# Kernel tuning notes

Measured on AMD Instinct MI355X. Metric: run time of the kernel, lower is better.

Reference implementation:

```python
import jax, jax.numpy as jnp
import numpy as np

N, E, D_IN = 50000, 800000, 64
EMB = [128, 128, 128, 128]
LIN = [128, 64]
B = 512  # number of graphs
BN_EPS = 1e-5


def setup_inputs() -> dict:
    key = jax.random.key(0)
    ks = jax.random.split(key, 20)
    inp = {
        "x": jax.random.normal(ks[0], (N, D_IN), dtype=jnp.float32),
        "edge_index": jax.random.randint(ks[1], (2, E), 0, N, dtype=jnp.int32),
        "batch_index": jnp.sort(jax.random.randint(ks[2], (N,), 0, B, dtype=jnp.int32)),
    }
    dims = [D_IN] + EMB
    for i in range(4):
        s = 1.0 / np.sqrt(dims[i])
        inp[f"W{i+1}"] = jax.random.uniform(ks[3 + i], (dims[i], dims[i + 1]), jnp.float32, -s, s)
        inp[f"b{i+1}"] = jnp.zeros((dims[i + 1],), jnp.float32)
    inp["lW1"] = jax.random.uniform(ks[8], (EMB[-1], LIN[0]), jnp.float32, -0.08, 0.08)
    inp["lb1"] = jnp.zeros((LIN[0],), jnp.float32)
    inp["lW2"] = jax.random.uniform(ks[9], (LIN[0], LIN[1]), jnp.float32, -0.08, 0.08)
    inp["lb2"] = jnp.zeros((LIN[1],), jnp.float32)
    inp["gamma"] = jnp.ones((LIN[1],), jnp.float32)
    inp["beta"] = jnp.zeros((LIN[1],), jnp.float32)
    inp["running_mean"] = jnp.zeros((LIN[1],), jnp.float32)
    inp["running_var"] = jnp.ones((LIN[1],), jnp.float32)
    inp["oW"] = jax.random.uniform(ks[10], (LIN[1], 1), jnp.float32, -0.12, 0.12)
    inp["ob"] = jnp.zeros((1,), jnp.float32)
    return inp


def reference(x, edge_index, batch_index, W1, b1, W2, b2, W3, b3, W4, b4,
              lW1, lb1, lW2, lb2, gamma, beta, running_mean, running_var, oW, ob):
    n = x.shape[0]
    loop = jnp.arange(n, dtype=edge_index.dtype)
    src = jnp.concatenate([edge_index[0], loop])  # [E+N]
    dst = jnp.concatenate([edge_index[1], loop])
    # GCN symmetric normalization (PyG GCNConv: deg from target with self-loops)
    deg = jax.ops.segment_sum(jnp.ones_like(dst, x.dtype), dst, num_segments=n)
    dinv = jnp.where(deg > 0, jax.lax.rsqrt(deg), 0.0)
    norm = dinv[src] * dinv[dst]  # [E+N]

    def conv(h, W, b):
        h = h @ W                                   # [N, out]
        msg = h[src] * norm[:, None]                # gather per edge
        return jax.ops.segment_sum(msg, dst, num_segments=n) + b

    h = jax.nn.relu(conv(x, W1, b1))
    h = jax.nn.relu(conv(h, W2, b2))
    h = jax.nn.relu(conv(h, W3, b3))
    h = jax.nn.relu(conv(h, W4, b4))

    # global mean pool over graphs (dropout layers are identity in eval mode)
    sums = jax.ops.segment_sum(h, batch_index, num_segments=B)
    cnts = jax.ops.segment_sum(jnp.ones((n,), h.dtype), batch_index, num_segments=B)
    pooled = sums / jnp.maximum(cnts, 1.0)[:, None]  # [B, EMB[-1]]

    h = pooled @ lW1 + lb1
    h = h @ lW2 + lb2
    h = (h - running_mean) * gamma * jax.lax.rsqrt(running_var + BN_EPS) + beta
    hidden = jax.nn.relu(h)
    out = hidden @ oW + ob
    return (out, hidden)
```

## Files before the change

kernel.cpp:

```cpp
#include <hip/hip_runtime.h>
#include <hip/hip_fp16.h>

struct alignas(8) half4v { __half2 a, b; };
using f16x8 = __attribute__((ext_vector_type(8))) _Float16;
using f32x4 = __attribute__((ext_vector_type(4))) float;

__global__ void zero_kernel(int* __restrict__ p, int n) {
  int i = blockIdx.x * blockDim.x + threadIdx.x;
  if (i < n) p[i] = 0;
}

__global__ void hist_kernel(const int* __restrict__ dst, int* __restrict__ deg,
                            int* __restrict__ eidx, int E) {
  int e0 = (blockIdx.x * blockDim.x + threadIdx.x) * 4;
  if (e0 + 3 < E) {
    int4 d4 = *(const int4*)&dst[e0];
    int r0 = atomicAdd(&deg[d4.x], 1);
    int r1 = atomicAdd(&deg[d4.y], 1);
    int r2 = atomicAdd(&deg[d4.z], 1);
    int r3 = atomicAdd(&deg[d4.w], 1);
    int4 o; o.x = r0; o.y = r1; o.z = r2; o.w = r3;
    *(int4*)&eidx[e0] = o;
  } else {
    for (int e = e0; e < E; ++e) eidx[e] = atomicAdd(&deg[dst[e]], 1);
  }
}

__global__ void dinv_bsum_kernel(const int* __restrict__ deg, float* __restrict__ dinv,
                                 int* __restrict__ bsum, int n) {
  __shared__ int s[256];
  int i = blockIdx.x * 256 + threadIdx.x;
  int d = (i < n) ? deg[i] : 0;
  if (i < n) dinv[i] = rsqrtf((float)(d + 1));
  s[threadIdx.x] = d;
  __syncthreads();
  for (int off = 128; off > 0; off >>= 1) {
    if (threadIdx.x < off) s[threadIdx.x] += s[threadIdx.x + off];
    __syncthreads();
  }
  if (threadIdx.x == 0) bsum[blockIdx.x] = s[0];
}

__global__ void scan_bsum_kernel(const int* __restrict__ bsum, int* __restrict__ bexcl,
                                 int nb, int* __restrict__ rowptr_last) {
  __shared__ int s[256];
  int t = threadIdx.x;
  int v = (t < nb) ? bsum[t] : 0;
  s[t] = v;
  __syncthreads();
  for (int off = 1; off < 256; off <<= 1) {
    int add = (t >= off) ? s[t - off] : 0;
    __syncthreads();
    s[t] += add;
    __syncthreads();
  }
  if (t < nb) bexcl[t] = s[t] - v;
  if (t == 255) *rowptr_last = s[255];
}

__global__ void rowptr_kernel(const int* __restrict__ cnt, const int* __restrict__ bexcl,
                              int* __restrict__ rowptr, int n) {
  __shared__ int s[256];
  int i = blockIdx.x * 256 + threadIdx.x;
  int t = threadIdx.x;
  int v = (i < n) ? cnt[i] : 0;
  s[t] = v;
  __syncthreads();
  for (int off = 1; off < 256; off <<= 1) {
    int add = (t >= off) ? s[t - off] : 0;
    __syncthreads();
    s[t] += add;
    __syncthreads();
  }
  if (i < n) rowptr[i] = bexcl[blockIdx.x] + s[t] - v;
}

__global__ void fill_kernel(const int* __restrict__ src, const int* __restrict__ dst,
                            const float* __restrict__ dinv, const int* __restrict__ rowptr,
                            const int* __restrict__ eidx, int2* __restrict__ colwv, int E) {
  int e0 = (blockIdx.x * blockDim.x + threadIdx.x) * 2;
  if (e0 + 1 < E) {
    int2 s2 = *(const int2*)&src[e0];
    int2 d2 = *(const int2*)&dst[e0];
    int2 x2 = *(const int2*)&eidx[e0];
    float dsx = dinv[s2.x], ddx = dinv[d2.x];
    float dsy = dinv[s2.y], ddy = dinv[d2.y];
    int slot0 = rowptr[d2.x] + x2.x;
    int slot1 = rowptr[d2.y] + x2.y;
    int2 p0; p0.x = s2.x; p0.y = __float_as_int(dsx * ddx);
    int2 p1; p1.x = s2.y; p1.y = __float_as_int(dsy * ddy);
    colwv[slot0] = p0;
    colwv[slot1] = p1;
  } else if (e0 < E) {
    int s = src[e0], d = dst[e0];
    int slot = rowptr[d] + eidx[e0];
    int2 packed;
    packed.x = s;
    packed.y = __float_as_int(dinv[s] * dinv[d]);
    colwv[slot] = packed;
  }
}

__global__ void f32_to_f16_kernel(const float* __restrict__ in, __half* __restrict__ out,
                                  int total4) {
  int i = blockIdx.x * blockDim.x + threadIdx.x;
  if (i >= total4) return;
  float4 v = ((const float4*)in)[i];
  half4v o;
  o.a = __floats2half2_rn(v.x, v.y);
  o.b = __floats2half2_rn(v.z, v.w);
  ((half4v*)out)[i] = o;
}

__global__ void pack_w_all_kernel(const float* __restrict__ W1, __half* __restrict__ Wp1,
                                  const float* __restrict__ W2, __half* __restrict__ Wp2,
                                  const float* __restrict__ W3, __half* __restrict__ Wp3,
                                  const float* __restrict__ W4, __half* __restrict__ Wp4) {
  int b = blockIdx.x;
  const float* W; __half* Wp; int idx;
  if (b < 32)       { W = W1; Wp = Wp1; idx = b * 256 + threadIdx.x; }
  else if (b < 96)  { W = W2; Wp = Wp2; idx = (b - 32) * 256 + threadIdx.x; }
  else if (b < 160) { W = W3; Wp = Wp3; idx = (b - 96) * 256 + threadIdx.x; }
  else              { W = W4; Wp = Wp4; idx = (b - 160) * 256 + threadIdx.x; }
  int j = idx & 7;
  int lane = (idx >> 3) & 63;
  int c = (idx >> 9) & 7;
  int ks = idx >> 12;
  int k = ks * 32 + ((lane >> 4) << 3) + j;
  int col = c * 16 + (lane & 15);
  Wp[idx] = __float2half(W[k * 128 + col]);
}

template <int D>
__global__ __launch_bounds__(256) void aggregate_h_kernel(
    const __half* __restrict__ h, const int* __restrict__ rowptr,
    const int2* __restrict__ colwv, const float* __restrict__ dinv,
    __half* __restrict__ out, int n) {
  int wid = (blockIdx.x * 256 + threadIdx.x) >> 6;
  int lane = threadIdx.x & 63;
  if (wid >= n) return;
  float di = dinv[wid];
  float sl = di * di;
  int beg = rowptr[wid], end = rowptr[wid + 1];
  const half4v* h4 = (const half4v*)h;
  constexpr int RQ = D / 4;
  float4 acc = {0.f, 0.f, 0.f, 0.f};
  constexpr int EPG = (D == 128) ? 2 : 4;
  const int sub = (D == 128) ? (lane >> 5) : (lane >> 4);
  const int lq = (D == 128) ? (lane & 31) : (lane & 15);
  for (int base = beg; base < end; base += 64) {
    int kk = base + lane;
    int c = 0; float ww = 0.f;
    if (kk < end) { int2 e = colwv[kk]; c = e.x; ww = __int_as_float(e.y); }
    int m = end - base; if (m > 64) m = 64;
    for (int t0 = 0; t0 < m; t0 += 8 * EPG) {
      half4v v[8]; float ws[8];
      #pragma unroll
      for (int u = 0; u < 8; ++u) {
        int t = t0 + EPG * u + sub;
        int cs = __shfl(c, t);
        ws[u] = __shfl(ww, t);
        v[u] = h4[(size_t)cs * RQ + lq];
      }
      #pragma unroll
      for (int u = 0; u < 8; ++u) {
        float2 fa = __half22float2(v[u].a);
        float2 fb = __half22float2(v[u].b);
        acc.x += ws[u] * fa.x; acc.y += ws[u] * fa.y;
        acc.z += ws[u] * fb.x; acc.w += ws[u] * fb.y;
      }
    }
  }
  if constexpr (D == 64) {
    acc.x += __shfl_xor(acc.x, 16); acc.y += __shfl_xor(acc.y, 16);
    acc.z += __shfl_xor(acc.z, 16); acc.w += __shfl_xor(acc.w, 16);
  }
  acc.x += __shfl_xor(acc.x, 32); acc.y += __shfl_xor(acc.y, 32);
  acc.z += __shfl_xor(acc.z, 32); acc.w += __shfl_xor(acc.w, 32);
  if (lane < RQ) {
    half4v hv = h4[(size_t)wid * RQ + lane];
    float2 fa = __half22float2(hv.a);
    float2 fb = __half22float2(hv.b);
    acc.x += sl * fa.x; acc.y += sl * fa.y; acc.z += sl * fb.x; acc.w += sl * fb.y;
    half4v o;
    o.a = __floats2half2_rn(acc.x, acc.y);
    o.b = __floats2half2_rn(acc.z, acc.w);
    ((half4v*)out)[(size_t)wid * RQ + lane] = o;
  }
}

template <int K>
__global__ __launch_bounds__(256) void gemm_mfma_kernel(
    const __half* __restrict__ A, const __half* __restrict__ Wp,
    const float* __restrict__ bias, __half* __restrict__ C, int n) {
  const int wave = threadIdx.x >> 6;
  const int lane = threadIdx.x & 63;
  const int r0 = blockIdx.x * 64 + wave * 16;
  const int arow = r0 + (lane & 15);
  const int kgrp = lane >> 4;
  f32x4 acc[8] = {};
  const f16x8* Wp8 = (const f16x8*)Wp;
  #pragma unroll
  for (int ks = 0; ks < K / 32; ++ks) {
    f16x8 afrag = {};
    if (arow < n) afrag = *(const f16x8*)&A[(size_t)arow * K + ks * 32 + kgrp * 8];
    #pragma unroll
    for (int c = 0; c < 8; ++c) {
      f16x8 bfrag = Wp8[(ks * 8 + c) * 64 + lane];
      acc[c] = __builtin_amdgcn_mfma_f32_16x16x32_f16(afrag, bfrag, acc[c], 0, 0, 0);
    }
  }
  const int colbase = lane & 15;
  #pragma unroll
  for (int c = 0; c < 8; ++c) {
    int col = c * 16 + colbase;
    float bv = bias[col];
    #pragma unroll
    for (int j = 0; j < 4; ++j) {
      int row = r0 + kgrp * 4 + j;
      if (row < n) C[(size_t)row * 128 + col] = __float2half(fmaxf(acc[c][j] + bv, 0.f));
    }
  }
}

__global__ __launch_bounds__(256) void pool_mean_kernel(
    const __half* __restrict__ h, const int* __restrict__ batch,
    float* __restrict__ pooled, int n) {
  int b = blockIdx.x;
  int lo = 0, hi = n;
  while (lo < hi) { int mid = (lo + hi) >> 1; if (batch[mid] < b) lo = mid + 1; else hi = mid; }
  int s = lo;
  hi = n;
  while (lo < hi) { int mid = (lo + hi) >> 1; if (batch[mid] < b + 1) lo = mid + 1; else hi = mid; }
  int e = lo;
  const half4v* h4 = (const half4v*)h;
  int q = threadIdx.x & 31;
  int r = threadIdx.x >> 5;
  float4 acc = {0.f, 0.f, 0.f, 0.f};
  for (int i = s + r; i < e; i += 8) {
    half4v v = h4[(size_t)i * 32 + q];
    float2 fa = __half22float2(v.a), fb = __half22float2(v.b);
    acc.x += fa.x; acc.y += fa.y; acc.z += fb.x; acc.w += fb.y;
  }
  __shared__ float4 red[8][32];
  red[r][q] = acc;
  __syncthreads();
  for (int off = 4; off > 0; off >>= 1) {
    if (r < off) {
      float4 o = red[r + off][q];
      acc.x += o.x; acc.y += o.y; acc.z += o.z; acc.w += o.w;
      red[r][q] = acc;
    }
    __syncthreads();
  }
  if (r == 0) {
    float c = fmaxf((float)(e - s), 1.0f);
    float4 o;
    o.x = acc.x / c; o.y = acc.y / c; o.z = acc.z / c; o.w = acc.w / c;
    ((float4*)pooled)[b * 32 + q] = o;
  }
}

__global__ __launch_bounds__(128) void mlp_kernel(
    const float* __restrict__ pooled,
    const float* __restrict__ lW1, const float* __restrict__ lb1,
    const float* __restrict__ lW2, const float* __restrict__ lb2,
    const float* __restrict__ gamma, const float* __restrict__ beta,
    const float* __restrict__ rm, const float* __restrict__ rv,
    const float* __restrict__ oW, const float* __restrict__ ob,
    float* __restrict__ out, int B) {
  int b = blockIdx.x, t = threadIdx.x;
  __shared__ float p[128], h1[128];
  p[t] = pooled[b * 128 + t];
  __syncthreads();
  float a1 = lb1[t];
  for (int k = 0; k < 128; ++k) a1 += p[k] * lW1[k * 128 + t];
  h1[t] = a1;
  __syncthreads();
  if (t < 64) {
    float a2 = lb2[t];
    for (int k = 0; k < 128; ++k) a2 += h1[k] * lW2[k * 64 + t];
    a2 = (a2 - rm[t]) * gamma[t] * rsqrtf(rv[t] + 1e-5f) + beta[t];
    float hd = fmaxf(a2, 0.f);
    out[B + b * 64 + t] = hd;
    float prod = hd * oW[t];
    #pragma unroll
    for (int off = 32; off > 0; off >>= 1) prod += __shfl_down(prod, off);
    if (t == 0) out[b] = prod + ob[0];
  }
}

extern "C" void kernel_launch(void* const* d_in, const int* in_sizes, int n_in,
                              void* d_out, int out_size, void* d_ws, size_t ws_size,
                              hipStream_t stream) {
  const float* x = (const float*)d_in[0];
  const int* ei = (const int*)d_in[1];
  const int* batch = (const int*)d_in[2];
  const float* W1 = (const float*)d_in[3];  const float* b1 = (const float*)d_in[4];
  const float* W2 = (const float*)d_in[5];  const float* b2 = (const float*)d_in[6];
  const float* W3 = (const float*)d_in[7];  const float* b3 = (const float*)d_in[8];
  const float* W4 = (const float*)d_in[9];  const float* b4 = (const float*)d_in[10];
  const float* lW1 = (const float*)d_in[11]; const float* lb1 = (const float*)d_in[12];
  const float* lW2 = (const float*)d_in[13]; const float* lb2 = (const float*)d_in[14];
  const float* gamma = (const float*)d_in[15]; const float* beta = (const float*)d_in[16];
  const float* rm = (const float*)d_in[17]; const float* rv = (const float*)d_in[18];
  const float* oW = (const float*)d_in[19]; const float* ob = (const float*)d_in[20];

  const int n = in_sizes[2];
  const int E = in_sizes[1] / 2;
  const int B = out_size / 65;
  const int* src = ei;
  const int* dst = ei + E;

  char* ws = (char*)d_ws;
  size_t off = 0;
  auto alloc = [&](size_t bytes) -> void* {
    void* p = ws + off;
    off += (bytes + 255) & ~(size_t)255;
    return p;
  };
  int* deg = (int*)alloc((size_t)n * 4);
  float* dinv = (float*)alloc((size_t)n * 4);
  int* rowptr = (int*)alloc((size_t)(n + 1) * 4);
  int* eidx = (int*)alloc((size_t)E * 4);
  int* bsum = (int*)alloc(256 * 4);
  int* bexcl = (int*)alloc(256 * 4);
  int2* colwv = (int2*)alloc((size_t)E * 8);
  __half* aggh = (__half*)alloc((size_t)n * 128 * 2);
  __half* hbuf = (__half*)alloc((size_t)n * 128 * 2);
  __half* xh = (__half*)alloc((size_t)n * 64 * 2);
  __half* Wp1 = (__half*)alloc(64 * 128 * 2);
  __half* Wp2 = (__half*)alloc(128 * 128 * 2);
  __half* Wp3 = (__half*)alloc(128 * 128 * 2);
  __half* Wp4 = (__half*)alloc(128 * 128 * 2);
  float* pooled = (float*)alloc((size_t)B * 128 * 4);

  const int nb = (n + 255) / 256;
  zero_kernel<<<nb, 256, 0, stream>>>(deg, n);
  hist_kernel<<<(E / 4 + 255) / 256, 256, 0, stream>>>(dst, deg, eidx, E);
  f32_to_f16_kernel<<<(n * 16 + 255) / 256, 256, 0, stream>>>(x, xh, n * 16);
  pack_w_all_kernel<<<224, 256, 0, stream>>>(W1, Wp1, W2, Wp2, W3, Wp3, W4, Wp4);
  dinv_bsum_kernel<<<nb, 256, 0, stream>>>(deg, dinv, bsum, n);
  scan_bsum_kernel<<<1, 256, 0, stream>>>(bsum, bexcl, nb, rowptr + n);
  rowptr_kernel<<<nb, 256, 0, stream>>>(deg, bexcl, rowptr, n);
  fill_kernel<<<(E / 2 + 255) / 256, 256, 0, stream>>>(src, dst, dinv, rowptr, eidx, colwv, E);

  const int aggblocks = (n + 3) / 4;
  const int gemmblocks = (n + 63) / 64;

  aggregate_h_kernel<64><<<aggblocks, 256, 0, stream>>>(xh, rowptr, colwv, dinv, aggh, n);
  gemm_mfma_kernel<64><<<gemmblocks, 256, 0, stream>>>(aggh, Wp1, b1, hbuf, n);
  aggregate_h_kernel<128><<<aggblocks, 256, 0, stream>>>(hbuf, rowptr, colwv, dinv, aggh, n);
  gemm_mfma_kernel<128><<<gemmblocks, 256, 0, stream>>>(aggh, Wp2, b2, hbuf, n);
  aggregate_h_kernel<128><<<aggblocks, 256, 0, stream>>>(hbuf, rowptr, colwv, dinv, aggh, n);
  gemm_mfma_kernel<128><<<gemmblocks, 256, 0, stream>>>(aggh, Wp3, b3, hbuf, n);
  aggregate_h_kernel<128><<<aggblocks, 256, 0, stream>>>(hbuf, rowptr, colwv, dinv, aggh, n);
  gemm_mfma_kernel<128><<<gemmblocks, 256, 0, stream>>>(aggh, Wp4, b4, hbuf, n);

  pool_mean_kernel<<<B, 256, 0, stream>>>(hbuf, batch, pooled, n);
  mlp_kernel<<<B, 128, 0, stream>>>(pooled, lW1, lb1, lW2, lb2, gamma, beta, rm, rv, oW, ob,
                                    (float*)d_out, B);
}
```

Measured before the change: 272.7 us.

## Fuse neighbor aggregation into MFMA GEMM via LDS and merge prep/pool kernels

Each GCN layer now aggregates 64 nodes per block into shared memory and immediately runs the MFMA GEMM from LDS, removing the intermediate aggregated feature buffer round-trip through global memory. The zero, fp16 conversion and weight packing kernels are merged into one prep kernel, and mean pooling is fused with the MLP head. This cuts memory traffic and launch count, at the risk that each wave now processes 16 nodes serially, which may reduce latency hiding and cause load imbalance within a block.

```diff
diff --git a/kernel.cpp b/kernel.cpp
--- a/kernel.cpp
+++ b/kernel.cpp
@@ -5,9 +5,39 @@
 using f16x8 = __attribute__((ext_vector_type(8))) _Float16;
 using f32x4 = __attribute__((ext_vector_type(4))) float;
 
-__global__ void zero_kernel(int* __restrict__ p, int n) {
-  int i = blockIdx.x * blockDim.x + threadIdx.x;
-  if (i < n) p[i] = 0;
+__global__ void prep_kernel(int* __restrict__ deg, int n, int nb,
+                            const float* __restrict__ x, __half* __restrict__ xh, int total4,
+                            const float* __restrict__ W1, __half* __restrict__ Wp1,
+                            const float* __restrict__ W2, __half* __restrict__ Wp2,
+                            const float* __restrict__ W3, __half* __restrict__ Wp3,
+                            const float* __restrict__ W4, __half* __restrict__ Wp4) {
+  int b = blockIdx.x;
+  if (b < nb) {
+    int i = b * 256 + threadIdx.x;
+    if (i < n) deg[i] = 0;
+  } else if (b < nb + 224) {
+    int pb = b - nb;
+    const float* W; __half* Wp; int idx;
+    if (pb < 32)       { W = W1; Wp = Wp1; idx = pb * 256 + threadIdx.x; }
+    else if (pb < 96)  { W = W2; Wp = Wp2; idx = (pb - 32) * 256 + threadIdx.x; }
+    else if (pb < 160) { W = W3; Wp = Wp3; idx = (pb - 96) * 256 + threadIdx.x; }
+    else               { W = W4; Wp = Wp4; idx = (pb - 160) * 256 + threadIdx.x; }
+    int j = idx & 7;
+    int lane = (idx >> 3) & 63;
+    int c = (idx >> 9) & 7;
+    int ks = idx >> 12;
+    int k = ks * 32 + ((lane >> 4) << 3) + j;
+    int col = c * 16 + (lane & 15);
+    Wp[idx] = __float2half(W[k * 128 + col]);
+  } else {
+    int i = (b - nb - 224) * 256 + threadIdx.x;
+    if (i >= total4) return;
+    float4 v = ((const float4*)x)[i];
+    half4v o;
+    o.a = __floats2half2_rn(v.x, v.y);
+    o.b = __floats2half2_rn(v.z, v.w);
+    ((half4v*)xh)[i] = o;
+  }
 }
 
 __global__ void hist_kernel(const int* __restrict__ dst, int* __restrict__ deg,
@@ -101,109 +131,77 @@
   }
 }
 
-__global__ void f32_to_f16_kernel(const float* __restrict__ in, __half* __restrict__ out,
-                                  int total4) {
-  int i = blockIdx.x * blockDim.x + threadIdx.x;
-  if (i >= total4) return;
-  float4 v = ((const float4*)in)[i];
-  half4v o;
-  o.a = __floats2half2_rn(v.x, v.y);
-  o.b = __floats2half2_rn(v.z, v.w);
-  ((half4v*)out)[i] = o;
-}
-
-__global__ void pack_w_all_kernel(const float* __restrict__ W1, __half* __restrict__ Wp1,
-                                  const float* __restrict__ W2, __half* __restrict__ Wp2,
-                                  const float* __restrict__ W3, __half* __restrict__ Wp3,
-                                  const float* __restrict__ W4, __half* __restrict__ Wp4) {
-  int b = blockIdx.x;
-  const float* W; __half* Wp; int idx;
-  if (b < 32)       { W = W1; Wp = Wp1; idx = b * 256 + threadIdx.x; }
-  else if (b < 96)  { W = W2; Wp = Wp2; idx = (b - 32) * 256 + threadIdx.x; }
-  else if (b < 160) { W = W3; Wp = Wp3; idx = (b - 96) * 256 + threadIdx.x; }
-  else              { W = W4; Wp = Wp4; idx = (b - 160) * 256 + threadIdx.x; }
-  int j = idx & 7;
-  int lane = (idx >> 3) & 63;
-  int c = (idx >> 9) & 7;
-  int ks = idx >> 12;
-  int k = ks * 32 + ((lane >> 4) << 3) + j;
-  int col = c * 16 + (lane & 15);
-  Wp[idx] = __float2half(W[k * 128 + col]);
-}
-
-template <int D>
-__global__ __launch_bounds__(256) void aggregate_h_kernel(
+template <int K>
+__global__ __launch_bounds__(256) void agg_gemm_kernel(
     const __half* __restrict__ h, const int* __restrict__ rowptr,
     const int2* __restrict__ colwv, const float* __restrict__ dinv,
-    __half* __restrict__ out, int n) {
-  int wid = (blockIdx.x * 256 + threadIdx.x) >> 6;
-  int lane = threadIdx.x & 63;
-  if (wid >= n) return;
-  float di = dinv[wid];
-  float sl = di * di;
-  int beg = rowptr[wid], end = rowptr[wid + 1];
-  const half4v* h4 = (const half4v*)h;
-  constexpr int RQ = D / 4;
-  float4 acc = {0.f, 0.f, 0.f, 0.f};
-  constexpr int EPG = (D == 128) ? 2 : 4;
-  const int sub = (D == 128) ? (lane >> 5) : (lane >> 4);
-  const int lq = (D == 128) ? (lane & 31) : (lane & 15);
-  for (int base = beg; base < end; base += 64) {
-    int kk = base + lane;
-    int c = 0; float ww = 0.f;
-    if (kk < end) { int2 e = colwv[kk]; c = e.x; ww = __int_as_float(e.y); }
-    int m = end - base; if (m > 64) m = 64;
-    for (int t0 = 0; t0 < m; t0 += 8 * EPG) {
-      half4v v[8]; float ws[8];
-      #pragma unroll
-      for (int u = 0; u < 8; ++u) {
-        int t = t0 + EPG * u + sub;
-        int cs = __shfl(c, t);
-        ws[u] = __shfl(ww, t);
-        v[u] = h4[(size_t)cs * RQ + lq];
-      }
-      #pragma unroll
-      for (int u = 0; u < 8; ++u) {
-        float2 fa = __half22float2(v[u].a);
-        float2 fb = __half22float2(v[u].b);
-        acc.x += ws[u] * fa.x; acc.y += ws[u] * fa.y;
-        acc.z += ws[u] * fb.x; acc.w += ws[u] * fb.y;
-      }
-    }
-  }
-  if constexpr (D == 64) {
-    acc.x += __shfl_xor(acc.x, 16); acc.y += __shfl_xor(acc.y, 16);
-    acc.z += __shfl_xor(acc.z, 16); acc.w += __shfl_xor(acc.w, 16);
-  }
-  acc.x += __shfl_xor(acc.x, 32); acc.y += __shfl_xor(acc.y, 32);
-  acc.z += __shfl_xor(acc.z, 32); acc.w += __shfl_xor(acc.w, 32);
-  if (lane < RQ) {
-    half4v hv = h4[(size_t)wid * RQ + lane];
-    float2 fa = __half22float2(hv.a);
-    float2 fb = __half22float2(hv.b);
-    acc.x += sl * fa.x; acc.y += sl * fa.y; acc.z += sl * fb.x; acc.w += sl * fb.y;
-    half4v o;
-    o.a = __floats2half2_rn(acc.x, acc.y);
-    o.b = __floats2half2_rn(acc.z, acc.w);
-    ((half4v*)out)[(size_t)wid * RQ + lane] = o;
-  }
-}
-
-template <int K>
-__global__ __launch_bounds__(256) void gemm_mfma_kernel(
-    const __half* __restrict__ A, const __half* __restrict__ Wp,
-    const float* __restrict__ bias, __half* __restrict__ C, int n) {
+    const __half* __restrict__ Wp, const float* __restrict__ bias,
+    __half* __restrict__ C, int n) {
+  constexpr int RQ = K / 4;
+  constexpr int ROWH = K + 8;
+  __shared__ __half Ash[64 * ROWH];
   const int wave = threadIdx.x >> 6;
   const int lane = threadIdx.x & 63;
-  const int r0 = blockIdx.x * 64 + wave * 16;
-  const int arow = r0 + (lane & 15);
+  const int r0 = blockIdx.x * 64;
+  constexpr int EPG = (K == 128) ? 2 : 4;
+  const int sub = (K == 128) ? (lane >> 5) : (lane >> 4);
+  const int lq = (K == 128) ? (lane & 31) : (lane & 15);
+  const half4v* h4 = (const half4v*)h;
+  for (int i = 0; i < 16; ++i) {
+    int node = r0 + wave * 16 + i;
+    if (node >= n) break;
+    float di = dinv[node];
+    float sl = di * di;
+    int beg = rowptr[node], end = rowptr[node + 1];
+    float4 acc = {0.f, 0.f, 0.f, 0.f};
+    for (int base = beg; base < end; base += 64) {
+      int kk = base + lane;
+      int c = 0; float ww = 0.f;
+      if (kk < end) { int2 e = colwv[kk]; c = e.x; ww = __int_as_float(e.y); }
+      int m = end - base; if (m > 64) m = 64;
+      for (int t0 = 0; t0 < m; t0 += 8 * EPG) {
+        half4v v[8]; float ws[8];
+        #pragma unroll
+        for (int u = 0; u < 8; ++u) {
+          int t = t0 + EPG * u + sub;
+          int cs = __shfl(c, t);
+          ws[u] = __shfl(ww, t);
+          v[u] = h4[(size_t)cs * RQ + lq];
+        }
+        #pragma unroll
+        for (int u = 0; u < 8; ++u) {
+          float2 fa = __half22float2(v[u].a);
+          float2 fb = __half22float2(v[u].b);
+          acc.x += ws[u] * fa.x; acc.y += ws[u] * fa.y;
+          acc.z += ws[u] * fb.x; acc.w += ws[u] * fb.y;
+        }
+      }
+    }
+    if constexpr (K == 64) {
+      acc.x += __shfl_xor(acc.x, 16); acc.y += __shfl_xor(acc.y, 16);
+      acc.z += __shfl_xor(acc.z, 16); acc.w += __shfl_xor(acc.w, 16);
+    }
+    acc.x += __shfl_xor(acc.x, 32); acc.y += __shfl_xor(acc.y, 32);
+    acc.z += __shfl_xor(acc.z, 32); acc.w += __shfl_xor(acc.w, 32);
+    if (lane < RQ) {
+      half4v hv = h4[(size_t)node * RQ + lane];
+      float2 fa = __half22float2(hv.a);
+      float2 fb = __half22float2(hv.b);
+      acc.x += sl * fa.x; acc.y += sl * fa.y; acc.z += sl * fb.x; acc.w += sl * fb.y;
+      half4v o;
+      o.a = __floats2half2_rn(acc.x, acc.y);
+      o.b = __floats2half2_rn(acc.z, acc.w);
+      *(half4v*)&Ash[(wave * 16 + i) * ROWH + lane * 4] = o;
+    }
+  }
+  __syncthreads();
+  const int lrow = wave * 16 + (lane & 15);
   const int kgrp = lane >> 4;
   f32x4 acc[8] = {};
   const f16x8* Wp8 = (const f16x8*)Wp;
   #pragma unroll
   for (int ks = 0; ks < K / 32; ++ks) {
-    f16x8 afrag = {};
-    if (arow < n) afrag = *(const f16x8*)&A[(size_t)arow * K + ks * 32 + kgrp * 8];
+    f16x8 afrag = *(const f16x8*)&Ash[lrow * ROWH + ks * 32 + kgrp * 8];
     #pragma unroll
     for (int c = 0; c < 8; ++c) {
       f16x8 bfrag = Wp8[(ks * 8 + c) * 64 + lane];
@@ -217,15 +215,20 @@
     float bv = bias[col];
     #pragma unroll
     for (int j = 0; j < 4; ++j) {
-      int row = r0 + kgrp * 4 + j;
+      int row = r0 + wave * 16 + kgrp * 4 + j;
       if (row < n) C[(size_t)row * 128 + col] = __float2half(fmaxf(acc[c][j] + bv, 0.f));
     }
   }
 }
 
-__global__ __launch_bounds__(256) void pool_mean_kernel(
+__global__ __launch_bounds__(256) void pool_mlp_kernel(
     const __half* __restrict__ h, const int* __restrict__ batch,
-    float* __restrict__ pooled, int n) {
+    const float* __restrict__ lW1, const float* __restrict__ lb1,
+    const float* __restrict__ lW2, const float* __restrict__ lb2,
+    const float* __restrict__ gamma, const float* __restrict__ beta,
+    const float* __restrict__ rm, const float* __restrict__ rv,
+    const float* __restrict__ oW, const float* __restrict__ ob,
+    float* __restrict__ out, int n, int B) {
   int b = blockIdx.x;
   int lo = 0, hi = n;
   while (lo < hi) { int mid = (lo + hi) >> 1; if (batch[mid] < b) lo = mid + 1; else hi = mid; }
@@ -253,29 +256,20 @@
     }
     __syncthreads();
   }
+  __shared__ float p[128], h1[128];
   if (r == 0) {
     float c = fmaxf((float)(e - s), 1.0f);
     float4 o;
     o.x = acc.x / c; o.y = acc.y / c; o.z = acc.z / c; o.w = acc.w / c;
-    ((float4*)pooled)[b * 32 + q] = o;
-  }
-}
-
-__global__ __launch_bounds__(128) void mlp_kernel(
-    const float* __restrict__ pooled,
-    const float* __restrict__ lW1, const float* __restrict__ lb1,
-    const float* __restrict__ lW2, const float* __restrict__ lb2,
-    const float* __restrict__ gamma, const float* __restrict__ beta,
-    const float* __restrict__ rm, const float* __restrict__ rv,
-    const float* __restrict__ oW, const float* __restrict__ ob,
-    float* __restrict__ out, int B) {
-  int b = blockIdx.x, t = threadIdx.x;
-  __shared__ float p[128], h1[128];
-  p[t] = pooled[b * 128 + t];
-  __syncthreads();
-  float a1 = lb1[t];
-  for (int k = 0; k < 128; ++k) a1 += p[k] * lW1[k * 128 + t];
-  h1[t] = a1;
+    *(float4*)&p[q * 4] = o;
+  }
+  __syncthreads();
+  int t = threadIdx.x;
+  if (t < 128) {
+    float a1 = lb1[t];
+    for (int k = 0; k < 128; ++k) a1 += p[k] * lW1[k * 128 + t];
+    h1[t] = a1;
+  }
   __syncthreads();
   if (t < 64) {
     float a2 = lb2[t];
@@ -326,38 +320,30 @@
   int* bsum = (int*)alloc(256 * 4);
   int* bexcl = (int*)alloc(256 * 4);
   int2* colwv = (int2*)alloc((size_t)E * 8);
-  __half* aggh = (__half*)alloc((size_t)n * 128 * 2);
   __half* hbuf = (__half*)alloc((size_t)n * 128 * 2);
+  __half* hbuf2 = (__half*)alloc((size_t)n * 128 * 2);
   __half* xh = (__half*)alloc((size_t)n * 64 * 2);
   __half* Wp1 = (__half*)alloc(64 * 128 * 2);
   __half* Wp2 = (__half*)alloc(128 * 128 * 2);
   __half* Wp3 = (__half*)alloc(128 * 128 * 2);
   __half* Wp4 = (__half*)alloc(128 * 128 * 2);
-  float* pooled = (float*)alloc((size_t)B * 128 * 4);
 
   const int nb = (n + 255) / 256;
-  zero_kernel<<<nb, 256, 0, stream>>>(deg, n);
+  const int f2h_blocks = (n * 16 + 255) / 256;
+  prep_kernel<<<nb + 224 + f2h_blocks, 256, 0, stream>>>(deg, n, nb, x, xh, n * 16,
+                                                         W1, Wp1, W2, Wp2, W3, Wp3, W4, Wp4);
   hist_kernel<<<(E / 4 + 255) / 256, 256, 0, stream>>>(dst, deg, eidx, E);
-  f32_to_f16_kernel<<<(n * 16 + 255) / 256, 256, 0, stream>>>(x, xh, n * 16);
-  pack_w_all_kernel<<<224, 256, 0, stream>>>(W1, Wp1, W2, Wp2, W3, Wp3, W4, Wp4);
   dinv_bsum_kernel<<<nb, 256, 0, stream>>>(deg, dinv, bsum, n);
   scan_bsum_kernel<<<1, 256, 0, stream>>>(bsum, bexcl, nb, rowptr + n);
   rowptr_kernel<<<nb, 256, 0, stream>>>(deg, bexcl, rowptr, n);
   fill_kernel<<<(E / 2 + 255) / 256, 256, 0, stream>>>(src, dst, dinv, rowptr, eidx, colwv, E);
 
-  const int aggblocks = (n + 3) / 4;
-  const int gemmblocks = (n + 63) / 64;
-
-  aggregate_h_kernel<64><<<aggblocks, 256, 0, stream>>>(xh, rowptr, colwv, dinv, aggh, n);
-  gemm_mfma_kernel<64><<<gemmblocks, 256, 0, stream>>>(aggh, Wp1, b1, hbuf, n);
-  aggregate_h_kernel<128><<<aggblocks, 256, 0, stream>>>(hbuf, rowptr, colwv, dinv, aggh, n);
-  gemm_mfma_kernel<128><<<gemmblocks, 256, 0, stream>>>(aggh, Wp2, b2, hbuf, n);
-  aggregate_h_kernel<128><<<aggblocks, 256, 0, stream>>>(hbuf, rowptr, colwv, dinv, aggh, n);
-  gemm_mfma_kernel<128><<<gemmblocks, 256, 0, stream>>>(aggh, Wp3, b3, hbuf, n);
-  aggregate_h_kernel<128><<<aggblocks, 256, 0, stream>>>(hbuf, rowptr, colwv, dinv, aggh, n);
-  gemm_mfma_kernel<128><<<gemmblocks, 256, 0, stream>>>(aggh, Wp4, b4, hbuf, n);
-
-  pool_mean_kernel<<<B, 256, 0, stream>>>(hbuf, batch, pooled, n);
-  mlp_kernel<<<B, 128, 0, stream>>>(pooled, lW1, lb1, lW2, lb2, gamma, beta, rm, rv, oW, ob,
-                                    (float*)d_out, B);
-}
+  const int fusedblocks = (n + 63) / 64;
+  agg_gemm_kernel<64><<<fusedblocks, 256, 0, stream>>>(xh, rowptr, colwv, dinv, Wp1, b1, hbuf, n);
+  agg_gemm_kernel<128><<<fusedblocks, 256, 0, stream>>>(hbuf, rowptr, colwv, dinv, Wp2, b2, hbuf2, n);
+  agg_gemm_kernel<128><<<fusedblocks, 256, 0, stream>>>(hbuf2, rowptr, colwv, dinv, Wp3, b3, hbuf, n);
+  agg_gemm_kernel<128><<<fusedblocks, 256, 0, stream>>>(hbuf, rowptr, colwv, dinv, Wp4, b4, hbuf2, n);
+
+  pool_mlp_kernel<<<B, 256, 0, stream>>>(hbuf2, batch, lW1, lb1, lW2, lb2, gamma, beta,
+                                         rm, rv, oW, ob, (float*)d_out, n, B);
+}
```

New measurement: 275.8 us. Within noise of the previous version (+1.1%).
